# Optimization experiments

Measured on AMD Instinct MI355X. Metric: run time of the kernel, lower is better.

## Reference

```python
import jax, jax.numpy as jnp
import numpy as np

N, D, R, NUM_HEADS = 8192, 256, 32, 4
ETA = 0.5


def setup_inputs() -> dict:
    key = jax.random.key(0)
    k_h, k_a, k_u = jax.random.split(key, 3)
    H = jax.random.normal(k_h, (N, D), dtype=jnp.float32)
    # sparse-ish symmetric adjacency with self loops (float mask, as in torch code)
    A = (jax.random.uniform(k_a, (N, N)) < 0.002).astype(jnp.float32)
    A = jnp.maximum(jnp.maximum(A, A.T), jnp.eye(N, dtype=jnp.float32))
    # symmetric normalized Laplacian L = I - D^{-1/2} A D^{-1/2}
    dinv = 1.0 / jnp.sqrt(A.sum(axis=1))
    L = jnp.eye(N, dtype=jnp.float32) - dinv[:, None] * A * dinv[None, :]
    # per-head orthonormal subspace bases U[k] in R^{D x R} (QR init as in module)
    raw = jax.random.normal(k_u, (NUM_HEADS, D, R), dtype=jnp.float32)
    U = jnp.linalg.qr(raw)[0]  # batched reduced QR -> [K, D, R]
    lambda_lap = jnp.asarray(0.1, dtype=jnp.float32)
    threshold = jnp.full((D,), 0.05, dtype=jnp.float32)
    return {"H": H, "adj_mask": A, "L": L, "U": U,
            "lambda_lap": lambda_lap, "threshold": threshold}


def reference(H, adj_mask, L, U, lambda_lap, threshold):
    n, d = H.shape
    K, _, r = U.shape
    scale = 1.0 / (r ** 0.5)
    neg = (1.0 - adj_mask) * -1e9  # additive graph mask, shared across heads

    Ht = H.T  # [d, n]
    agg = jnp.zeros_like(Ht)
    for k in range(K):  # small fixed head loop (keeps one [n,n] block live at a time)
        Uk = U[k]                      # [d, r]
        Zk = Uk.T @ Ht                 # [r, n]
        scores = (Zk.T @ Zk) * scale + neg  # [n, n]
        alpha = jax.nn.softmax(scores, axis=1)
        agg = agg + Uk @ (Zk @ alpha.T)     # [d, n]

    lap_grad = lambda_lap * (L @ H)        # [n, d]
    H_half = (Ht + ETA * agg).T - ETA * lap_grad
    # proximal soft-threshold (proj is None since in_dim == out_dim)
    H_out = jnp.sign(H_half) * jax.nn.relu(jnp.abs(H_half) - threshold[None, :])

    # orthogonality regularizer over all head pairs
    G = jnp.einsum('kdr,lds->klrs', U, U)  # [K, K, r, r] (small)
    I = jnp.eye(r, dtype=U.dtype)
    diag_loss = ((G[jnp.arange(K), jnp.arange(K)] - I) ** 2).sum()
    upper = jnp.triu(jnp.ones((K, K), dtype=U.dtype), 1)
    off_loss = ((G ** 2).sum(axis=(2, 3)) * upper).sum()
    orth_loss = diag_loss + off_loss

    lap_smooth = jnp.sum(H_out * (L @ H_out))  # trace(H_out^T L H_out)
    return H_out, orth_loss, lap_smooth
```

## Files before the change

kernel.cpp:

```cpp
#include <hip/hip_runtime.h>
#include <hip/hip_bf16.h>
#include <math.h>

#define NN 8192
#define DD 256
#define RR 32
#define KH 4
#define PP 128
#define CAP 128
#define CAPL 128
#define NSTASH 64
#define ETA 0.5f
#define SCALE 0.17677669529663687f

__device__ __forceinline__ unsigned short f2bf(float f) {
  union { float f; unsigned u; } v; v.f = f;
  unsigned r = v.u + 0x7fffu + ((v.u >> 16) & 1u);
  return (unsigned short)(r >> 16);
}
__device__ __forceinline__ float bflo(unsigned u) { return __uint_as_float(u << 16); }
__device__ __forceinline__ float bfhi(unsigned u) { return __uint_as_float(u & 0xffff0000u); }

__global__ __launch_bounds__(256) void zgemm_scan(const float* __restrict__ A,
                                                  const float* __restrict__ H,
                                                  const float* __restrict__ U,
                                                  float* __restrict__ B2,
                                                  unsigned short* __restrict__ Zb,
                                                  unsigned short* __restrict__ Hb,
                                                  float* __restrict__ orth_part,
                                                  int* __restrict__ lowCols,
                                                  int* __restrict__ lowCnt,
                                                  int* __restrict__ upCols,
                                                  int* __restrict__ upCnt) {
  __shared__ float smem[5152];
  int tid = threadIdx.x;
  int bx = blockIdx.x;
  int lane = tid & 63, wv = tid >> 6;

  if (bx >= 650) {
    int row = (NN - 1) - (bx - 650);
    const float* a = A + (size_t)row * NN;
    __shared__ int wsum2[4];
    __shared__ int sbase;
    if (tid == 0) sbase = 0;
    int nch = (row >> 10) + 1;
    for (int c = 0; c < nch; ++c) {
      int g0 = c * 1024 + tid * 4;
      float4 x = *(const float4*)(a + g0);
      int m0 = (g0 + 0 < row) && (x.x != 0.f);
      int m1 = (g0 + 1 < row) && (x.y != 0.f);
      int m2 = (g0 + 2 < row) && (x.z != 0.f);
      int m3 = (g0 + 3 < row) && (x.w != 0.f);
      int cnt = m0 + m1 + m2 + m3;
      int incl = cnt;
#pragma unroll
      for (int off = 1; off < 64; off <<= 1) {
        int t = __shfl_up(incl, off);
        if (lane >= off) incl += t;
      }
      if (lane == 63) wsum2[wv] = incl;
      __syncthreads();
      int base = sbase;
#pragma unroll
      for (int w = 0; w < 4; ++w) if (w < wv) base += wsum2[w];
      int o = base + incl - cnt;
      int chunkTot = wsum2[0] + wsum2[1] + wsum2[2] + wsum2[3];
      if (m0) { int col = g0 + 0; if (o < CAPL) { lowCols[(size_t)row * CAPL + o] = col; int s = atomicAdd(&upCnt[col], 1); if (s < CAPL) upCols[(size_t)col * CAPL + s] = row; } o++; }
      if (m1) { int col = g0 + 1; if (o < CAPL) { lowCols[(size_t)row * CAPL + o] = col; int s = atomicAdd(&upCnt[col], 1); if (s < CAPL) upCols[(size_t)col * CAPL + s] = row; } o++; }
      if (m2) { int col = g0 + 2; if (o < CAPL) { lowCols[(size_t)row * CAPL + o] = col; int s = atomicAdd(&upCnt[col], 1); if (s < CAPL) upCols[(size_t)col * CAPL + s] = row; } o++; }
      if (m3) { int col = g0 + 3; if (o < CAPL) { lowCols[(size_t)row * CAPL + o] = col; int s = atomicAdd(&upCnt[col], 1); if (s < CAPL) upCols[(size_t)col * CAPL + s] = row; } o++; }
      __syncthreads();
      if (tid == 0) sbase = base + chunkTot;
    }
    __syncthreads();
    if (tid == 0) lowCnt[row] = sbase;
    return;
  }
  if (bx >= 394) {
    int base = (bx - 394) * 8192;
#pragma unroll
    for (int q = 0; q < 8; ++q) {
      int idx = base + q * 1024 + tid * 4;
      float4 v = *(const float4*)(H + idx);
      uint2 p;
      p.x = (unsigned)f2bf(v.x) | ((unsigned)f2bf(v.y) << 16);
      p.y = (unsigned)f2bf(v.z) | ((unsigned)f2bf(v.w) << 16);
      *(uint2*)(Hb + idx) = p;
    }
    return;
  }
  if (bx >= 266) {
    int idx = (bx - 266) * 256 + tid;
    int k = idx / (DD * RR);
    int rem = idx % (DD * RR);
    int d = rem / RR;
    int r = rem % RR;
    B2[(k * RR + r) * DD + d] = U[idx];
    return;
  }
  if (bx >= 256) {
    int bid = bx - 256;
    int b = bid, k = 0;
    while (b >= (KH - k)) { b -= (KH - k); k++; }
    int l = k + b;
    float* redo = smem;
    const float* uk = U + (size_t)k * DD * RR;
    const float* ul = U + (size_t)l * DD * RR;
    float acc = 0.f;
#pragma unroll
    for (int q = 0; q < 4; ++q) {
      int e = tid * 4 + q;
      int r = e >> 5, s2 = e & 31;
      float g = 0.f;
      for (int d = 0; d < DD; ++d) g += uk[d * RR + r] * ul[d * RR + s2];
      if (k == l) {
        float c3 = g - (r == s2 ? 1.f : 0.f);
        acc += c3 * c3;
      } else {
        acc += g * g;
      }
    }
    redo[tid] = acc;
    __syncthreads();
    for (int off = 128; off > 0; off >>= 1) {
      if (tid < off) redo[tid] += redo[tid + off];
      __syncthreads();
    }
    if (tid == 0) orth_part[bid] = redo[0];
    return;
  }
  float* As = smem;
  float* Bs = smem + 1056;
  int r0 = bx * 32;
  int tx = tid & 15, ty = tid >> 4;
  int cx = tx * 8, ry = ty * 2;
  float acc[2][8];
#pragma unroll
  for (int i = 0; i < 2; ++i)
#pragma unroll
    for (int j = 0; j < 8; ++j) acc[i][j] = 0.f;

  for (int k0 = 0; k0 < DD; k0 += 32) {
    {
      int r = tid >> 3;
      int kc = (tid & 7) * 4;
      float4 x = *(const float4*)(H + (size_t)(r0 + r) * DD + k0 + kc);
      As[(kc + 0) * 33 + r] = x.x; As[(kc + 1) * 33 + r] = x.y;
      As[(kc + 2) * 33 + r] = x.z; As[(kc + 3) * 33 + r] = x.w;
    }
#pragma unroll
    for (int q = 0; q < 4; ++q) {
      int f = tid + 256 * q;
      int kk = f >> 5, pc = (f & 31) * 4;
      *(float4*)(&Bs[kk * 128 + pc]) =
          *(const float4*)(U + (size_t)(pc >> 5) * DD * RR + (size_t)(k0 + kk) * RR + (pc & 31));
    }
    __syncthreads();
#pragma unroll
    for (int kk = 0; kk < 32; ++kk) {
      float av[2];
      av[0] = As[kk * 33 + ry]; av[1] = As[kk * 33 + ry + 1];
      float bv[8];
      *(float4*)(bv) = *(const float4*)(&Bs[kk * 128 + cx]);
      *(float4*)(bv + 4) = *(const float4*)(&Bs[kk * 128 + cx + 4]);
#pragma unroll
      for (int i = 0; i < 2; ++i)
#pragma unroll
        for (int j = 0; j < 8; ++j) acc[i][j] += av[i] * bv[j];
    }
    __syncthreads();
  }
#pragma unroll
  for (int i = 0; i < 2; ++i) {
    uint4 p;
    p.x = (unsigned)f2bf(acc[i][0]) | ((unsigned)f2bf(acc[i][1]) << 16);
    p.y = (unsigned)f2bf(acc[i][2]) | ((unsigned)f2bf(acc[i][3]) << 16);
    p.z = (unsigned)f2bf(acc[i][4]) | ((unsigned)f2bf(acc[i][5]) << 16);
    p.w = (unsigned)f2bf(acc[i][6]) | ((unsigned)f2bf(acc[i][7]) << 16);
    *(uint4*)(Zb + (size_t)(r0 + ry + i) * PP + cx) = p;
  }
}

__global__ __launch_bounds__(256) void csr_attn(const unsigned short* __restrict__ Zb,
                                                const int* __restrict__ lowCols,
                                                const int* __restrict__ lowCnt,
                                                const int* __restrict__ upCols,
                                                const int* __restrict__ upCnt,
                                                int* __restrict__ cols,
                                                int* __restrict__ nnzArr,
                                                float* __restrict__ dinv,
                                                float* __restrict__ aggZ) {
  int row = blockIdx.x;
  int tid = threadIdx.x;
  int lane = tid & 63, wv = tid >> 6;
  __shared__ int scols[CAP];
  __shared__ int utmp[CAPL];
  __shared__ float zi[PP];
  __shared__ unsigned short zzb[NSTASH][130];
  __shared__ float alpha[KH][CAP];
  __shared__ float2 redp[4][64];

  if (tid < PP) zi[tid] = bflo((unsigned)Zb[(size_t)row * PP + tid]);

  int lcT = lowCnt[row];
  int ucT = upCnt[row];
  int lc = lcT < (CAP - 1) ? lcT : (CAP - 1);
  for (int t = tid; t < lc; t += 256) scols[t] = lowCols[(size_t)row * CAPL + t];
  if (tid == 0) scols[lc] = row;
  int ucR = ucT < CAPL ? ucT : CAPL;
  for (int t = tid; t < ucR; t += 256) utmp[t] = upCols[(size_t)row * CAPL + t];
  __syncthreads();
  for (int t = tid; t < ucR; t += 256) {
    int e = utmp[t], r = 0;
    for (int q = 0; q < ucR; ++q) r += (utmp[q] < e);
    int pos = lc + 1 + r;
    if (pos < CAP) scols[pos] = e;
  }
  int total = lcT + 1 + ucT;
  int nn = total < CAP ? total : CAP;
  if (tid == 0) {
    nnzArr[row] = nn;
    dinv[row] = 1.0f / sqrtf((float)total);
  }
  __syncthreads();
  for (int t = tid; t < nn; t += 256) cols[(size_t)row * CAP + t] = scols[t];

  int ns = nn < NSTASH ? nn : NSTASH;
  for (int j = wv; j < ns; j += 4) {
    unsigned x = *(const unsigned*)(Zb + (size_t)scols[j] * PP + lane * 2);
    *(unsigned*)(&zzb[j][lane * 2]) = x;
  }
  __syncthreads();

  {
    int k = wv;
    float s0 = -1e30f, s1 = -1e30f;
    if (lane < nn) {
      const unsigned short* zs = &zzb[lane][k * RR];
      float acc = 0.f;
#pragma unroll
      for (int r = 0; r < RR; r += 4) {
        float4 aa = *(const float4*)(zi + k * RR + r);
        unsigned u0 = *(const unsigned*)(zs + r);
        unsigned u1 = *(const unsigned*)(zs + r + 2);
        acc += aa.x * bflo(u0) + aa.y * bfhi(u0) + aa.z * bflo(u1) + aa.w * bfhi(u1);
      }
      s0 = acc * SCALE;
    }
    int j1 = lane + 64;
    if (j1 < nn) {
      const unsigned short* zj = Zb + (size_t)scols[j1] * PP + k * RR;
      float acc = 0.f;
#pragma unroll
      for (int r = 0; r < RR; r += 4) {
        float4 aa = *(const float4*)(zi + k * RR + r);
        unsigned u0 = *(const unsigned*)(zj + r);
        unsigned u1 = *(const unsigned*)(zj + r + 2);
        acc += aa.x * bflo(u0) + aa.y * bfhi(u0) + aa.z * bflo(u1) + aa.w * bfhi(u1);
      }
      s1 = acc * SCALE;
    }
    float m = fmaxf(s0, s1);
#pragma unroll
    for (int off = 32; off > 0; off >>= 1) m = fmaxf(m, __shfl_xor(m, off));
    float e0 = (lane < nn) ? expf(s0 - m) : 0.f;
    float e1 = (j1 < nn) ? expf(s1 - m) : 0.f;
    float s = e0 + e1;
#pragma unroll
    for (int off = 32; off > 0; off >>= 1) s += __shfl_xor(s, off);
    float inv = 1.0f / s;
    if (lane < nn) alpha[k][lane] = e0 * inv;
    if (j1 < nn) alpha[k][j1] = e1 * inv;
  }
  __syncthreads();

  {
    int c2 = tid & 63, hf = tid >> 6;
    int hd = c2 >> 4;
    float a0 = 0.f, a1 = 0.f;
    for (int jj = hf; jj < nn; jj += 4) {
      unsigned u;
      if (jj < NSTASH) u = *(const unsigned*)(&zzb[jj][c2 * 2]);
      else u = *(const unsigned*)(Zb + (size_t)scols[jj] * PP + c2 * 2);
      float al = alpha[hd][jj];
      a0 += al * bflo(u);
      a1 += al * bfhi(u);
    }
    redp[hf][c2] = make_float2(a0, a1);
  }
  __syncthreads();
  if (tid < 64) {
    float2 r0 = redp[0][tid], r1 = redp[1][tid], r2 = redp[2][tid], r3 = redp[3][tid];
    float2 s2 = make_float2(r0.x + r1.x + r2.x + r3.x, r0.y + r1.y + r2.y + r3.y);
    *(float2*)(aggZ + (size_t)row * PP + tid * 2) = s2;
  }
}

__global__ __launch_bounds__(256) void sgather(const unsigned short* __restrict__ Hb,
                                               const int* __restrict__ cols,
                                               const int* __restrict__ nnzArr,
                                               const float* __restrict__ dinv,
                                               float* __restrict__ S) {
  int row = blockIdx.x;
  int tid = threadIdx.x;
  int lane = tid & 63, wv = tid >> 6;
  __shared__ int scols[CAP];
  __shared__ float sdinv[CAP];
  __shared__ float sred[4][260];
  int nn = nnzArr[row];
  if (tid < nn) {
    int c = cols[(size_t)row * CAP + tid];
    scols[tid] = c;
    sdinv[tid] = dinv[c];
  }
  __syncthreads();
  float4 acc = make_float4(0.f, 0.f, 0.f, 0.f);
  for (int jj = wv; jj < nn; jj += 4) {
    uint2 u = *(const uint2*)(Hb + (size_t)scols[jj] * DD + lane * 4);
    float w = sdinv[jj];
    acc.x += w * bflo(u.x); acc.y += w * bfhi(u.x);
    acc.z += w * bflo(u.y); acc.w += w * bfhi(u.y);
  }
  *(float4*)(&sred[wv][lane * 4]) = acc;
  __syncthreads();
  float s = sred[0][tid] + sred[1][tid] + sred[2][tid] + sred[3][tid];
  S[(size_t)row * DD + tid] = s;
}

__global__ __launch_bounds__(256) void egemm(const float* __restrict__ A,
                                             const float* __restrict__ B,
                                             const float* __restrict__ Hm,
                                             const float* __restrict__ S,
                                             const float* __restrict__ dinv,
                                             const float* __restrict__ thr,
                                             const float* __restrict__ lambda_p,
                                             float* __restrict__ out,
                                             unsigned short* __restrict__ Houtb) {
  __shared__ float As[32][33];
  __shared__ float Bs[32][128];
  int tid = threadIdx.x;
  int r0 = blockIdx.x * 32;
  int c0 = blockIdx.y * 128;
  int tx = tid & 15, ty = tid >> 4;
  int cx = tx * 8, ry = ty * 2;
  float acc[2][8];
#pragma unroll
  for (int i = 0; i < 2; ++i)
#pragma unroll
    for (int j = 0; j < 8; ++j) acc[i][j] = 0.f;

  for (int k0 = 0; k0 < PP; k0 += 32) {
    {
      int r = tid >> 3;
      int kc = (tid & 7) * 4;
      float4 x = *(const float4*)(A + (size_t)(r0 + r) * PP + k0 + kc);
      As[kc + 0][r] = x.x; As[kc + 1][r] = x.y; As[kc + 2][r] = x.z; As[kc + 3][r] = x.w;
    }
#pragma unroll
    for (int q = 0; q < 4; ++q) {
      int f = tid + 256 * q;
      int kk = f >> 5, pc = (f & 31) * 4;
      *(float4*)(&Bs[kk][pc]) = *(const float4*)(B + (size_t)(k0 + kk) * DD + c0 + pc);
    }
    __syncthreads();
#pragma unroll
    for (int kk = 0; kk < 32; ++kk) {
      float av[2];
      av[0] = As[kk][ry]; av[1] = As[kk][ry + 1];
      float bv[8];
      *(float4*)(bv) = *(const float4*)(&Bs[kk][cx]);
      *(float4*)(bv + 4) = *(const float4*)(&Bs[kk][cx + 4]);
#pragma unroll
      for (int i = 0; i < 2; ++i)
#pragma unroll
        for (int j = 0; j < 8; ++j) acc[i][j] += av[i] * bv[j];
    }
    __syncthreads();
  }
  float lam = lambda_p[0];
  int gc = c0 + cx;
  float4 t0 = *(const float4*)(thr + gc);
  float4 t1 = *(const float4*)(thr + gc + 4);
#pragma unroll
  for (int i = 0; i < 2; ++i) {
    int gr = r0 + ry + i;
    float dv = dinv[gr];
    float4 h0 = *(const float4*)(Hm + (size_t)gr * DD + gc);
    float4 h1 = *(const float4*)(Hm + (size_t)gr * DD + gc + 4);
    float4 s0 = *(const float4*)(S + (size_t)gr * DD + gc);
    float4 s1 = *(const float4*)(S + (size_t)gr * DD + gc + 4);
    float hv[8] = {h0.x, h0.y, h0.z, h0.w, h1.x, h1.y, h1.z, h1.w};
    float sv[8] = {s0.x, s0.y, s0.z, s0.w, s1.x, s1.y, s1.z, s1.w};
    float tv[8] = {t0.x, t0.y, t0.z, t0.w, t1.x, t1.y, t1.z, t1.w};
    float ov[8];
#pragma unroll
    for (int j = 0; j < 8; ++j) {
      float val = hv[j] + ETA * acc[i][j] - ETA * lam * (hv[j] - dv * sv[j]);
      float av = fabsf(val) - tv[j];
      ov[j] = (av > 0.f) ? copysignf(av, val) : 0.f;
    }
    *(float4*)(out + (size_t)gr * DD + gc) = make_float4(ov[0], ov[1], ov[2], ov[3]);
    *(float4*)(out + (size_t)gr * DD + gc + 4) = make_float4(ov[4], ov[5], ov[6], ov[7]);
    uint4 p;
    p.x = (unsigned)f2bf(ov[0]) | ((unsigned)f2bf(ov[1]) << 16);
    p.y = (unsigned)f2bf(ov[2]) | ((unsigned)f2bf(ov[3]) << 16);
    p.z = (unsigned)f2bf(ov[4]) | ((unsigned)f2bf(ov[5]) << 16);
    p.w = (unsigned)f2bf(ov[6]) | ((unsigned)f2bf(ov[7]) << 16);
    *(uint4*)(Houtb + (size_t)gr * DD + gc) = p;
  }
}

__global__ __launch_bounds__(256) void lap_rows(const float* __restrict__ Hout,
                                                const unsigned short* __restrict__ Houtb,
                                                const int* __restrict__ cols,
                                                const int* __restrict__ nnzArr,
                                                const float* __restrict__ dinv,
                                                float* __restrict__ part) {
  int row = blockIdx.x;
  int tid = threadIdx.x;
  int lane = tid & 63, wv = tid >> 6;
  __shared__ int scols[CAP];
  __shared__ float sdinv[CAP];
  __shared__ float sred[4][260];
  int nn = nnzArr[row];
  if (tid < nn) {
    int c = cols[(size_t)row * CAP + tid];
    scols[tid] = c;
    sdinv[tid] = dinv[c];
  }
  __syncthreads();
  float4 acc = make_float4(0.f, 0.f, 0.f, 0.f);
  for (int jj = wv; jj < nn; jj += 4) {
    uint2 u = *(const uint2*)(Houtb + (size_t)scols[jj] * DD + lane * 4);
    float w = sdinv[jj];
    acc.x += w * bflo(u.x); acc.y += w * bfhi(u.x);
    acc.z += w * bflo(u.y); acc.w += w * bfhi(u.y);
  }
  *(float4*)(&sred[wv][lane * 4]) = acc;
  __syncthreads();
  if (wv == 0) {
    float4 s4;
    s4.x = sred[0][lane * 4 + 0] + sred[1][lane * 4 + 0] + sred[2][lane * 4 + 0] + sred[3][lane * 4 + 0];
    s4.y = sred[0][lane * 4 + 1] + sred[1][lane * 4 + 1] + sred[2][lane * 4 + 1] + sred[3][lane * 4 + 1];
    s4.z = sred[0][lane * 4 + 2] + sred[1][lane * 4 + 2] + sred[2][lane * 4 + 2] + sred[3][lane * 4 + 2];
    s4.w = sred[0][lane * 4 + 3] + sred[1][lane * 4 + 3] + sred[2][lane * 4 + 3] + sred[3][lane * 4 + 3];
    float4 h4 = *(const float4*)(Hout + (size_t)row * DD + lane * 4);
    float dvr = dinv[row];
    float val = h4.x * (h4.x - dvr * s4.x) + h4.y * (h4.y - dvr * s4.y) +
                h4.z * (h4.z - dvr * s4.z) + h4.w * (h4.w - dvr * s4.w);
#pragma unroll
    for (int off = 32; off > 0; off >>= 1) val += __shfl_xor(val, off);
    if (lane == 0) part[row] = val;
  }
}

__global__ __launch_bounds__(256) void finalize(const float* __restrict__ lap_part,
                                                const float* __restrict__ orth_part,
                                                float* __restrict__ out) {
  __shared__ double red[256];
  int tid = threadIdx.x;
  double s = 0.0;
  for (int i = tid; i < NN; i += 256) s += (double)lap_part[i];
  red[tid] = s;
  __syncthreads();
  for (int off = 128; off > 0; off >>= 1) {
    if (tid < off) red[tid] += red[tid + off];
    __syncthreads();
  }
  if (tid == 0) {
    double o = 0.0;
    for (int i = 0; i < 10; ++i) o += (double)orth_part[i];
    out[(size_t)NN * DD] = (float)o;
    out[(size_t)NN * DD + 1] = (float)red[0];
  }
}

extern "C" void kernel_launch(void* const* d_in, const int* in_sizes, int n_in,
                              void* d_out, int out_size, void* d_ws, size_t ws_size,
                              hipStream_t stream) {
  const float* H = (const float*)d_in[0];
  const float* A = (const float*)d_in[1];
  const float* U = (const float*)d_in[3];
  const float* lambda_p = (const float*)d_in[4];
  const float* thr = (const float*)d_in[5];
  float* out = (float*)d_out;

  char* w = (char*)d_ws;
  float* B2 = (float*)w;             w += (size_t)PP * DD * 4;
  int* cols = (int*)w;               w += (size_t)NN * CAP * 4;
  int* lowCols = (int*)w;            w += (size_t)NN * CAPL * 4;
  int* upCols = (int*)w;             w += (size_t)NN * CAPL * 4;
  int* lowCnt = (int*)w;             w += (size_t)NN * 4;
  int* upCnt = (int*)w;              w += (size_t)NN * 4;
  int* nnzArr = (int*)w;             w += (size_t)NN * 4;
  float* dinv = (float*)w;           w += (size_t)NN * 4;
  unsigned short* Zb = (unsigned short*)w;   w += (size_t)NN * PP * 2;
  unsigned short* Hb = (unsigned short*)w;   w += (size_t)NN * DD * 2;
  unsigned short* Houtb = (unsigned short*)w; w += (size_t)NN * DD * 2;
  float* aggZ = (float*)w;           w += (size_t)NN * PP * 4;
  float* S = (float*)w;              w += (size_t)NN * DD * 4;
  float* lap_part = (float*)w;       w += (size_t)NN * 4;
  float* orth_part = (float*)w;      w += 64;

  hipMemsetAsync(upCnt, 0, (size_t)NN * 4, stream);
  zgemm_scan<<<dim3(650 + NN), dim3(256), 0, stream>>>(A, H, U, B2, Zb, Hb, orth_part,
                                                       lowCols, lowCnt, upCols, upCnt);
  csr_attn<<<dim3(NN), dim3(256), 0, stream>>>(Zb, lowCols, lowCnt, upCols, upCnt,
                                               cols, nnzArr, dinv, aggZ);
  sgather<<<dim3(NN), dim3(256), 0, stream>>>(Hb, cols, nnzArr, dinv, S);
  egemm<<<dim3(NN / 32, 2), dim3(256), 0, stream>>>(aggZ, B2, H, S, dinv, thr, lambda_p,
                                                    out, Houtb);
  lap_rows<<<dim3(NN), dim3(256), 0, stream>>>(out, Houtb, cols, nnzArr, dinv, lap_part);
  finalize<<<dim3(1), dim3(256), 0, stream>>>(lap_part, orth_part, out);
}
```

Measured before the change: 159.9 us.

## Fuse neighbor gather into CSR attention and use symmetric half-neighbors for Laplacian

The S = D^-1/2 A D^-1/2 H gather is folded into the CSR attention kernel, so the separate sgather launch and the cols/nnzArr round-trip through global memory go away. Neighbor degrees are recomputed from the low/up counts rather than read from a dinv array written by another block. The Laplacian quadratic form now visits only lower-triangle neighbors with a doubled weight, using symmetry, and adds the self-loop term analytically. The Z stash shrinks to 48 rows to make room in shared memory, so more attention score reads hit global memory.

```diff
diff --git a/kernel.cpp b/kernel.cpp
--- a/kernel.cpp
+++ b/kernel.cpp
@@ -9,7 +9,7 @@
 #define PP 128
 #define CAP 128
 #define CAPL 128
-#define NSTASH 64
+#define NSTASH 48
 #define ETA 0.5f
 #define SCALE 0.17677669529663687f
 
@@ -181,15 +181,15 @@
   }
 }
 
-__global__ __launch_bounds__(256) void csr_attn(const unsigned short* __restrict__ Zb,
-                                                const int* __restrict__ lowCols,
-                                                const int* __restrict__ lowCnt,
-                                                const int* __restrict__ upCols,
-                                                const int* __restrict__ upCnt,
-                                                int* __restrict__ cols,
-                                                int* __restrict__ nnzArr,
-                                                float* __restrict__ dinv,
-                                                float* __restrict__ aggZ) {
+__global__ __launch_bounds__(256) void csr_attn_s(const unsigned short* __restrict__ Zb,
+                                                  const unsigned short* __restrict__ Hb,
+                                                  const int* __restrict__ lowCols,
+                                                  const int* __restrict__ lowCnt,
+                                                  const int* __restrict__ upCols,
+                                                  const int* __restrict__ upCnt,
+                                                  float* __restrict__ dinv,
+                                                  float* __restrict__ aggZ,
+                                                  float* __restrict__ S) {
   int row = blockIdx.x;
   int tid = threadIdx.x;
   int lane = tid & 63, wv = tid >> 6;
@@ -197,8 +197,8 @@
   __shared__ int utmp[CAPL];
   __shared__ float zi[PP];
   __shared__ unsigned short zzb[NSTASH][130];
-  __shared__ float alpha[KH][CAP];
-  __shared__ float2 redp[4][64];
+  __shared__ float sdinv[CAP];
+  __shared__ float uni[1024];
 
   if (tid < PP) zi[tid] = bflo((unsigned)Zb[(size_t)row * PP + tid]);
 
@@ -218,17 +218,35 @@
   }
   int total = lcT + 1 + ucT;
   int nn = total < CAP ? total : CAP;
-  if (tid == 0) {
-    nnzArr[row] = nn;
-    dinv[row] = 1.0f / sqrtf((float)total);
-  }
-  __syncthreads();
-  for (int t = tid; t < nn; t += 256) cols[(size_t)row * CAP + t] = scols[t];
-
-  int ns = nn < NSTASH ? nn : NSTASH;
-  for (int j = wv; j < ns; j += 4) {
-    unsigned x = *(const unsigned*)(Zb + (size_t)scols[j] * PP + lane * 2);
-    *(unsigned*)(&zzb[j][lane * 2]) = x;
+  if (tid == 0) dinv[row] = 1.0f / sqrtf((float)total);
+  __syncthreads();
+
+  if (tid < nn) {
+    int c = scols[tid];
+    int cc = lowCnt[c] + 1 + upCnt[c];
+    sdinv[tid] = 1.0f / sqrtf((float)cc);
+  }
+  __syncthreads();
+
+  {
+    float4 acc = make_float4(0.f, 0.f, 0.f, 0.f);
+    for (int jj = wv; jj < nn; jj += 4) {
+      int c = scols[jj];
+      if (jj < NSTASH) {
+        unsigned x = *(const unsigned*)(Zb + (size_t)c * PP + lane * 2);
+        *(unsigned*)(&zzb[jj][lane * 2]) = x;
+      }
+      uint2 u = *(const uint2*)(Hb + (size_t)c * DD + lane * 4);
+      float w = sdinv[jj];
+      acc.x += w * bflo(u.x); acc.y += w * bfhi(u.x);
+      acc.z += w * bflo(u.y); acc.w += w * bfhi(u.y);
+    }
+    *(float4*)(&uni[wv * 256 + lane * 4]) = acc;
+  }
+  __syncthreads();
+  {
+    float s = uni[0 * 256 + tid] + uni[1 * 256 + tid] + uni[2 * 256 + tid] + uni[3 * 256 + tid];
+    S[(size_t)row * DD + tid] = s;
   }
   __syncthreads();
 
@@ -236,14 +254,25 @@
     int k = wv;
     float s0 = -1e30f, s1 = -1e30f;
     if (lane < nn) {
-      const unsigned short* zs = &zzb[lane][k * RR];
       float acc = 0.f;
-#pragma unroll
-      for (int r = 0; r < RR; r += 4) {
-        float4 aa = *(const float4*)(zi + k * RR + r);
-        unsigned u0 = *(const unsigned*)(zs + r);
-        unsigned u1 = *(const unsigned*)(zs + r + 2);
-        acc += aa.x * bflo(u0) + aa.y * bfhi(u0) + aa.z * bflo(u1) + aa.w * bfhi(u1);
+      if (lane < NSTASH) {
+        const unsigned short* zs = &zzb[lane][k * RR];
+#pragma unroll
+        for (int r = 0; r < RR; r += 4) {
+          float4 aa = *(const float4*)(zi + k * RR + r);
+          unsigned u0 = *(const unsigned*)(zs + r);
+          unsigned u1 = *(const unsigned*)(zs + r + 2);
+          acc += aa.x * bflo(u0) + aa.y * bfhi(u0) + aa.z * bflo(u1) + aa.w * bfhi(u1);
+        }
+      } else {
+        const unsigned short* zj = Zb + (size_t)scols[lane] * PP + k * RR;
+#pragma unroll
+        for (int r = 0; r < RR; r += 4) {
+          float4 aa = *(const float4*)(zi + k * RR + r);
+          unsigned u0 = *(const unsigned*)(zj + r);
+          unsigned u1 = *(const unsigned*)(zj + r + 2);
+          acc += aa.x * bflo(u0) + aa.y * bfhi(u0) + aa.z * bflo(u1) + aa.w * bfhi(u1);
+        }
       }
       s0 = acc * SCALE;
     }
@@ -269,8 +298,8 @@
 #pragma unroll
     for (int off = 32; off > 0; off >>= 1) s += __shfl_xor(s, off);
     float inv = 1.0f / s;
-    if (lane < nn) alpha[k][lane] = e0 * inv;
-    if (j1 < nn) alpha[k][j1] = e1 * inv;
+    if (lane < nn) uni[k * CAP + lane] = e0 * inv;
+    if (j1 < nn) uni[k * CAP + j1] = e1 * inv;
   }
   __syncthreads();
 
@@ -282,49 +311,21 @@
       unsigned u;
       if (jj < NSTASH) u = *(const unsigned*)(&zzb[jj][c2 * 2]);
       else u = *(const unsigned*)(Zb + (size_t)scols[jj] * PP + c2 * 2);
-      float al = alpha[hd][jj];
+      float al = uni[hd * CAP + jj];
       a0 += al * bflo(u);
       a1 += al * bfhi(u);
     }
-    redp[hf][c2] = make_float2(a0, a1);
+    *(float2*)(&uni[512 + hf * 128 + c2 * 2]) = make_float2(a0, a1);
   }
   __syncthreads();
   if (tid < 64) {
-    float2 r0 = redp[0][tid], r1 = redp[1][tid], r2 = redp[2][tid], r3 = redp[3][tid];
+    float2 r0 = *(float2*)(&uni[512 + 0 * 128 + tid * 2]);
+    float2 r1 = *(float2*)(&uni[512 + 1 * 128 + tid * 2]);
+    float2 r2 = *(float2*)(&uni[512 + 2 * 128 + tid * 2]);
+    float2 r3 = *(float2*)(&uni[512 + 3 * 128 + tid * 2]);
     float2 s2 = make_float2(r0.x + r1.x + r2.x + r3.x, r0.y + r1.y + r2.y + r3.y);
     *(float2*)(aggZ + (size_t)row * PP + tid * 2) = s2;
   }
-}
-
-__global__ __launch_bounds__(256) void sgather(const unsigned short* __restrict__ Hb,
-                                               const int* __restrict__ cols,
-                                               const int* __restrict__ nnzArr,
-                                               const float* __restrict__ dinv,
-                                               float* __restrict__ S) {
-  int row = blockIdx.x;
-  int tid = threadIdx.x;
-  int lane = tid & 63, wv = tid >> 6;
-  __shared__ int scols[CAP];
-  __shared__ float sdinv[CAP];
-  __shared__ float sred[4][260];
-  int nn = nnzArr[row];
-  if (tid < nn) {
-    int c = cols[(size_t)row * CAP + tid];
-    scols[tid] = c;
-    sdinv[tid] = dinv[c];
-  }
-  __syncthreads();
-  float4 acc = make_float4(0.f, 0.f, 0.f, 0.f);
-  for (int jj = wv; jj < nn; jj += 4) {
-    uint2 u = *(const uint2*)(Hb + (size_t)scols[jj] * DD + lane * 4);
-    float w = sdinv[jj];
-    acc.x += w * bflo(u.x); acc.y += w * bfhi(u.x);
-    acc.z += w * bflo(u.y); acc.w += w * bfhi(u.y);
-  }
-  *(float4*)(&sred[wv][lane * 4]) = acc;
-  __syncthreads();
-  float s = sred[0][tid] + sred[1][tid] + sred[2][tid] + sred[3][tid];
-  S[(size_t)row * DD + tid] = s;
 }
 
 __global__ __launch_bounds__(256) void egemm(const float* __restrict__ A,
@@ -412,25 +413,26 @@
 
 __global__ __launch_bounds__(256) void lap_rows(const float* __restrict__ Hout,
                                                 const unsigned short* __restrict__ Houtb,
-                                                const int* __restrict__ cols,
-                                                const int* __restrict__ nnzArr,
+                                                const int* __restrict__ lowCols,
+                                                const int* __restrict__ lowCnt,
                                                 const float* __restrict__ dinv,
                                                 float* __restrict__ part) {
-  int row = blockIdx.x;
+  int row = (NN - 1) - blockIdx.x;
   int tid = threadIdx.x;
   int lane = tid & 63, wv = tid >> 6;
-  __shared__ int scols[CAP];
-  __shared__ float sdinv[CAP];
+  __shared__ int scols[CAPL];
+  __shared__ float sdinv[CAPL];
   __shared__ float sred[4][260];
-  int nn = nnzArr[row];
-  if (tid < nn) {
-    int c = cols[(size_t)row * CAP + tid];
+  int lcT = lowCnt[row];
+  int lc = lcT < CAPL ? lcT : CAPL;
+  if (tid < lc) {
+    int c = lowCols[(size_t)row * CAPL + tid];
     scols[tid] = c;
-    sdinv[tid] = dinv[c];
+    sdinv[tid] = 2.0f * dinv[c];
   }
   __syncthreads();
   float4 acc = make_float4(0.f, 0.f, 0.f, 0.f);
-  for (int jj = wv; jj < nn; jj += 4) {
+  for (int jj = wv; jj < lc; jj += 4) {
     uint2 u = *(const uint2*)(Houtb + (size_t)scols[jj] * DD + lane * 4);
     float w = sdinv[jj];
     acc.x += w * bflo(u.x); acc.y += w * bfhi(u.x);
@@ -446,8 +448,9 @@
     s4.w = sred[0][lane * 4 + 3] + sred[1][lane * 4 + 3] + sred[2][lane * 4 + 3] + sred[3][lane * 4 + 3];
     float4 h4 = *(const float4*)(Hout + (size_t)row * DD + lane * 4);
     float dvr = dinv[row];
-    float val = h4.x * (h4.x - dvr * s4.x) + h4.y * (h4.y - dvr * s4.y) +
-                h4.z * (h4.z - dvr * s4.z) + h4.w * (h4.w - dvr * s4.w);
+    float own = 1.0f - dvr * dvr;
+    float val = h4.x * (own * h4.x - dvr * s4.x) + h4.y * (own * h4.y - dvr * s4.y) +
+                h4.z * (own * h4.z - dvr * s4.z) + h4.w * (own * h4.w - dvr * s4.w);
 #pragma unroll
     for (int off = 32; off > 0; off >>= 1) val += __shfl_xor(val, off);
     if (lane == 0) part[row] = val;
@@ -487,12 +490,10 @@
 
   char* w = (char*)d_ws;
   float* B2 = (float*)w;             w += (size_t)PP * DD * 4;
-  int* cols = (int*)w;               w += (size_t)NN * CAP * 4;
   int* lowCols = (int*)w;            w += (size_t)NN * CAPL * 4;
   int* upCols = (int*)w;             w += (size_t)NN * CAPL * 4;
   int* lowCnt = (int*)w;             w += (size_t)NN * 4;
   int* upCnt = (int*)w;              w += (size_t)NN * 4;
-  int* nnzArr = (int*)w;             w += (size_t)NN * 4;
   float* dinv = (float*)w;           w += (size_t)NN * 4;
   unsigned short* Zb = (unsigned short*)w;   w += (size_t)NN * PP * 2;
   unsigned short* Hb = (unsigned short*)w;   w += (size_t)NN * DD * 2;
@@ -505,11 +506,10 @@
   hipMemsetAsync(upCnt, 0, (size_t)NN * 4, stream);
   zgemm_scan<<<dim3(650 + NN), dim3(256), 0, stream>>>(A, H, U, B2, Zb, Hb, orth_part,
                                                        lowCols, lowCnt, upCols, upCnt);
-  csr_attn<<<dim3(NN), dim3(256), 0, stream>>>(Zb, lowCols, lowCnt, upCols, upCnt,
-                                               cols, nnzArr, dinv, aggZ);
-  sgather<<<dim3(NN), dim3(256), 0, stream>>>(Hb, cols, nnzArr, dinv, S);
+  csr_attn_s<<<dim3(NN), dim3(256), 0, stream>>>(Zb, Hb, lowCols, lowCnt, upCols, upCnt,
+                                                 dinv, aggZ, S);
   egemm<<<dim3(NN / 32, 2), dim3(256), 0, stream>>>(aggZ, B2, H, S, dinv, thr, lambda_p,
                                                     out, Houtb);
-  lap_rows<<<dim3(NN), dim3(256), 0, stream>>>(out, Houtb, cols, nnzArr, dinv, lap_part);
+  lap_rows<<<dim3(NN), dim3(256), 0, stream>>>(out, Houtb, lowCols, lowCnt, dinv, lap_part);
   finalize<<<dim3(1), dim3(256), 0, stream>>>(lap_part, orth_part, out);
 }
```

Result: faster. 152.6 us (-4.6%).
